# Kernel optimization log

Hardware: AMD Instinct MI355X
Metric: run time of the kernel (lower is better)

## Reference

```python
import jax, jax.numpy as jnp
import numpy as np

D_K = 64

def setup_inputs() -> dict:
    key = jax.random.key(0)
    kq, kk, kv, km = jax.random.split(key, 4)
    B, H, S, D = 8, 8, 1024, D_K
    Q = jax.random.normal(kq, (B, H, S, D), dtype=jnp.float32)
    K = jax.random.normal(kk, (B, H, S, D), dtype=jnp.float32)
    V = jax.random.normal(kv, (B, H, S, D), dtype=jnp.float32)
    attention_masks = (jax.random.uniform(km, (B, 1, 1, S)) > 0.1).astype(jnp.float32)
    return {"Q": Q, "K": K, "V": V, "attention_masks": attention_masks}

def reference(Q, K, V, attention_masks):
    # scores = exp(QK^T / sqrt(d_k))  -- raw exp, NO max-subtraction (faithful to source)
    scale = 1.0 / np.sqrt(D_K).astype(np.float32)
    scores = jnp.exp(jnp.einsum('bhqd,bhkd->bhqk', Q, K) * scale)
    scores = scores * attention_masks  # multiplicative masking
    attention_scores = scores / (jnp.sum(scores, axis=-1, keepdims=True) + 1e-8)
    context = jnp.einsum('bhqk,bhkd->bhqd', attention_scores, V)
    return (context, attention_scores)
```

## Files before the change

### kernel.cpp

```cpp
#include <hip/hip_runtime.h>


typedef float    f32x4 __attribute__((ext_vector_type(4)));
typedef _Float16 f16x8 __attribute__((ext_vector_type(8)));
typedef _Float16 f16x4 __attribute__((ext_vector_type(4)));

#define MFMA32(A, B, C) __builtin_amdgcn_mfma_f32_16x16x32_f16((A), (B), (C), 0, 0, 0)
#define MFMA16(A, B, C) __builtin_amdgcn_mfma_f32_16x16x16f16((A), (B), (C), 0, 0, 0)

#define BHN 64
#define SEQ 1024
#define DIM 64

__device__ inline f16x8 cvt8(f32x4 a, f32x4 b) {
    f16x8 r;
    r[0] = (_Float16)a[0]; r[1] = (_Float16)a[1]; r[2] = (_Float16)a[2]; r[3] = (_Float16)a[3];
    r[4] = (_Float16)b[0]; r[5] = (_Float16)b[1]; r[6] = (_Float16)b[2]; r[7] = (_Float16)b[3];
    return r;
}

__global__ __launch_bounds__(256)
void cvt_kv(const float* __restrict__ K, const float* __restrict__ V,
            _Float16* __restrict__ Kh, _Float16* __restrict__ VTP)
{
    __shared__ _Float16 tile[128 * 65];
    const int bh = blockIdx.x >> 3;
    const int kc = blockIdx.x & 7;
    const int t  = threadIdx.x;
    const size_t base = ((size_t)bh * SEQ + (size_t)kc * 128) * DIM;

    for (int it = 0; it < 8; ++it) {
        int idx = it * 256 + t;
        int key = idx >> 4;
        int c4  = idx & 15;
        f32x4 kv = *(const f32x4*)(K + base + key * DIM + c4 * 4);
        f32x4 vv = *(const f32x4*)(V + base + key * DIM + c4 * 4);
        f16x4 kh4;
        kh4[0] = (_Float16)kv[0]; kh4[1] = (_Float16)kv[1];
        kh4[2] = (_Float16)kv[2]; kh4[3] = (_Float16)kv[3];
        *(f16x4*)(Kh + base + key * DIM + c4 * 4) = kh4;
        tile[key * 65 + c4 * 4 + 0] = (_Float16)vv[0];
        tile[key * 65 + c4 * 4 + 1] = (_Float16)vv[1];
        tile[key * 65 + c4 * 4 + 2] = (_Float16)vv[2];
        tile[key * 65 + c4 * 4 + 3] = (_Float16)vv[3];
    }
    __syncthreads();
    for (int it = 0; it < 8; ++it) {
        int flat = it * 256 + t;
        int ktl  = flat >> 8;
        int rem  = flat & 255;
        int l    = rem >> 2;
        int c    = rem & 3;
        f16x4 o;
        #pragma unroll
        for (int j = 0; j < 4; ++j)
            o[j] = tile[(ktl * 16 + ((l >> 4) << 2) + j) * 65 + c * 16 + (l & 15)];
        *(f16x4*)(VTP + (((size_t)bh * 64 + kc * 8 + ktl) * 64 + l) * 16 + c * 4) = o;
    }
}

template <bool PRECONV>
__global__ __launch_bounds__(256, 2)
void attn_main(const float* __restrict__ Q, const float* __restrict__ K,
               const float* __restrict__ V, const float* __restrict__ mask,
               const _Float16* __restrict__ Kh, const _Float16* __restrict__ VTP,
               float* __restrict__ ctx, float* __restrict__ scores)
{
    __shared__ _Float16 Et[32 * 1024];

    const int bid = blockIdx.x;
    const int wg  = ((bid & 7) << 8) | (bid >> 3);
    const int bh  = wg >> 5;
    const int qb  = wg & 31;
    const int b   = bh >> 3;
    const int w    = threadIdx.x >> 6;
    const int lane = threadIdx.x & 63;
    const int col  = lane & 15;
    const int g    = lane >> 4;
    const int q0   = qb * 32;
    const int kb   = w * 256;
    const float scale = 0.125f;
    char* EtB = (char*)Et;

    f16x8 qf[2][2];
    {
        const float* qbase = Q + ((size_t)bh * SEQ + q0) * DIM;
        #pragma unroll
        for (int s = 0; s < 2; ++s)
            #pragma unroll
            for (int f = 0; f < 2; ++f) {
                const float* p = qbase + (s * 16 + col) * DIM + f * 32 + g * 8;
                qf[s][f] = cvt8(*(const f32x4*)p, *(const f32x4*)(p + 4));
            }
    }
    const float* mb = mask + (size_t)b * SEQ + kb;
    const _Float16* kbase = Kh + ((size_t)bh * SEQ + kb + col) * DIM + g * 8;
    const _Float16* vtpb  = VTP + (((size_t)bh * 64 + w * 16) * 64 + lane) * 16;

    f32x4 cacc[2][4];
    #pragma unroll
    for (int s = 0; s < 2; ++s)
        #pragma unroll
        for (int dt = 0; dt < 4; ++dt) cacc[s][dt] = (f32x4){0.f, 0.f, 0.f, 0.f};

    f16x8 k0, k1, va, vb;
    f32x4 m4;
    if (PRECONV) {
        k0 = *(const f16x8*)(kbase);
        k1 = *(const f16x8*)(kbase + 32);
        va = *(const f16x8*)(vtpb);
        vb = *(const f16x8*)(vtpb + 8);
    } else {
        const float* kp = K + ((size_t)bh * SEQ + kb + col) * DIM + g * 8;
        k0 = cvt8(*(const f32x4*)kp,        *(const f32x4*)(kp + 4));
        k1 = cvt8(*(const f32x4*)(kp + 32), *(const f32x4*)(kp + 36));
        #pragma unroll
        for (int e = 0; e < 8; ++e) {
            va[e] = (_Float16)V[((size_t)bh * SEQ + kb + g * 4 + (e & 3)) * DIM + (e >> 2) * 16 + col];
            vb[e] = (_Float16)V[((size_t)bh * SEQ + kb + g * 4 + (e & 3)) * DIM + (2 + (e >> 2)) * 16 + col];
        }
    }
    m4 = *(const f32x4*)(mb + g * 4);

    for (int kt = 0; kt < 16; ++kt) {
        const int ktn = (kt + 1) & 15;
        f16x8 n0, n1, nva, nvb;
        if (PRECONV) {
            n0  = *(const f16x8*)(kbase + (size_t)ktn * 16 * DIM);
            n1  = *(const f16x8*)(kbase + (size_t)ktn * 16 * DIM + 32);
            nva = *(const f16x8*)(vtpb + (size_t)ktn * 64 * 16);
            nvb = *(const f16x8*)(vtpb + (size_t)ktn * 64 * 16 + 8);
        } else {
            const float* kp = K + ((size_t)bh * SEQ + kb + ktn * 16 + col) * DIM + g * 8;
            n0 = cvt8(*(const f32x4*)kp,        *(const f32x4*)(kp + 4));
            n1 = cvt8(*(const f32x4*)(kp + 32), *(const f32x4*)(kp + 36));
            #pragma unroll
            for (int e = 0; e < 8; ++e) {
                nva[e] = (_Float16)V[((size_t)bh * SEQ + kb + ktn * 16 + g * 4 + (e & 3)) * DIM + (e >> 2) * 16 + col];
                nvb[e] = (_Float16)V[((size_t)bh * SEQ + kb + ktn * 16 + g * 4 + (e & 3)) * DIM + (2 + (e >> 2)) * 16 + col];
            }
        }
        f32x4 nm = *(const f32x4*)(mb + ktn * 16 + g * 4);

        f16x4 pf[2];
        #pragma unroll
        for (int s = 0; s < 2; ++s) {
            f32x4 acc = {0.f, 0.f, 0.f, 0.f};
            acc = MFMA32(k0, qf[s][0], acc);
            acc = MFMA32(k1, qf[s][1], acc);
            f16x4 eh;
            eh[0] = (_Float16)(__expf(acc[0] * scale) * m4[0]);
            eh[1] = (_Float16)(__expf(acc[1] * scale) * m4[1]);
            eh[2] = (_Float16)(__expf(acc[2] * scale) * m4[2]);
            eh[3] = (_Float16)(__expf(acc[3] * scale) * m4[3]);
            pf[s] = eh;
            const int row = s * 16 + col;
            const int kg  = (w * 64 + kt * 4 + g) ^ ((row & 3) << 2);
            *(f16x4*)(EtB + row * 2048 + kg * 8) = eh;
        }
        {
            f16x4 vt0 = __builtin_shufflevector(va, va, 0, 1, 2, 3);
            f16x4 vt1 = __builtin_shufflevector(va, va, 4, 5, 6, 7);
            f16x4 vt2 = __builtin_shufflevector(vb, vb, 0, 1, 2, 3);
            f16x4 vt3 = __builtin_shufflevector(vb, vb, 4, 5, 6, 7);
            cacc[0][0] = MFMA16(vt0, pf[0], cacc[0][0]);
            cacc[1][0] = MFMA16(vt0, pf[1], cacc[1][0]);
            cacc[0][1] = MFMA16(vt1, pf[0], cacc[0][1]);
            cacc[1][1] = MFMA16(vt1, pf[1], cacc[1][1]);
            cacc[0][2] = MFMA16(vt2, pf[0], cacc[0][2]);
            cacc[1][2] = MFMA16(vt2, pf[1], cacc[1][2]);
            cacc[0][3] = MFMA16(vt3, pf[0], cacc[0][3]);
            cacc[1][3] = MFMA16(vt3, pf[1], cacc[1][3]);
        }
        k0 = n0; k1 = n1; va = nva; vb = nvb; m4 = nm;
    }

    __syncthreads();

    const int r0 = w * 8;
    float* srow = scores + ((size_t)bh * SEQ + q0) * SEQ;
    for (int j = 0; j < 8; ++j) {
        const int r = r0 + j;
        f16x4 ev[4];
        #pragma unroll
        for (int q = 0; q < 4; ++q) {
            const int kg = (q * 64 + lane) ^ ((r & 3) << 2);
            ev[q] = *(const f16x4*)(EtB + r * 2048 + kg * 8);
        }
        float s0 = 0.f;
        #pragma unroll
        for (int q = 0; q < 4; ++q)
            #pragma unroll
            for (int i = 0; i < 4; ++i) s0 += (float)ev[q][i];
        #pragma unroll
        for (int off = 1; off < 64; off <<= 1) s0 += __shfl_xor(s0, off, 64);
        const float invr = 1.0f / (s0 + 1e-8f);
        float* dst = srow + (size_t)r * SEQ + lane * 4;
        #pragma unroll
        for (int q = 0; q < 4; ++q) {
            f32x4 o;
            o[0] = (float)ev[q][0] * invr;
            o[1] = (float)ev[q][1] * invr;
            o[2] = (float)ev[q][2] * invr;
            o[3] = (float)ev[q][3] * invr;
            __builtin_nontemporal_store(o, (f32x4*)(dst + q * 256));
        }
        if (lane == 0) *(float*)(EtB + r0 * 2048 + j * 4) = invr;
    }

    __syncthreads();

    if (w != 0) {
        float* dump = (float*)(EtB + (1 + (w - 1) * 8) * 2048);
        #pragma unroll
        for (int s = 0; s < 2; ++s)
            #pragma unroll
            for (int dt = 0; dt < 4; ++dt)
                #pragma unroll
                for (int i = 0; i < 4; ++i)
                    dump[((s * 4 + dt) * 4 + i) * 64 + lane] = cacc[s][dt][i];
    }
    __syncthreads();
    if (w == 0) {
        #pragma unroll
        for (int s = 0; s < 2; ++s) {
            const int qrow = s * 16 + col;
            const float invr = *(const float*)(EtB + (qrow >> 3) * 8 * 2048 + (qrow & 7) * 4);
            #pragma unroll
            for (int dt = 0; dt < 4; ++dt) {
                f32x4 r = cacc[s][dt];
                #pragma unroll
                for (int ww = 1; ww < 4; ++ww) {
                    const float* dump = (const float*)(EtB + (1 + (ww - 1) * 8) * 2048);
                    #pragma unroll
                    for (int i = 0; i < 4; ++i)
                        r[i] += dump[((s * 4 + dt) * 4 + i) * 64 + lane];
                }
                r[0] *= invr; r[1] *= invr; r[2] *= invr; r[3] *= invr;
                *(f32x4*)(ctx + ((size_t)bh * SEQ + q0 + qrow) * DIM + dt * 16 + g * 4) = r;
            }
        }
    }
}

extern "C" void kernel_launch(void* const* d_in, const int* in_sizes, int n_in,
                              void* d_out, int out_size, void* d_ws, size_t ws_size,
                              hipStream_t stream)
{
    const float* Q    = (const float*)d_in[0];
    const float* K    = (const float*)d_in[1];
    const float* V    = (const float*)d_in[2];
    const float* mask = (const float*)d_in[3];
    float* ctx    = (float*)d_out;
    float* scores = ctx + (size_t)BHN * SEQ * DIM;

    const size_t elems = (size_t)BHN * SEQ * DIM;
    const size_t need  = elems * 2 * sizeof(_Float16);
    if (ws_size >= need) {
        _Float16* Kh  = (_Float16*)d_ws;
        _Float16* VTP = Kh + elems;
        cvt_kv<<<512, 256, 0, stream>>>(K, V, Kh, VTP);
        attn_main<true><<<2048, 256, 0, stream>>>(Q, K, V, mask, Kh, VTP, ctx, scores);
    } else {
        attn_main<false><<<2048, 256, 0, stream>>>(Q, K, V, mask, nullptr, nullptr, ctx, scores);
    }
}
```

Before: 100.9 us.

## Give each wave full key range for 16 query rows, keep scores in registers

```diff
diff --git a/kernel.cpp b/kernel.cpp
--- a/kernel.cpp
+++ b/kernel.cpp
@@ -66,42 +66,34 @@
                const _Float16* __restrict__ Kh, const _Float16* __restrict__ VTP,
                float* __restrict__ ctx, float* __restrict__ scores)
 {
-    __shared__ _Float16 Et[32 * 1024];
-
     const int bid = blockIdx.x;
-    const int wg  = ((bid & 7) << 8) | (bid >> 3);
-    const int bh  = wg >> 5;
-    const int qb  = wg & 31;
+    const int wg  = ((bid & 7) << 7) | (bid >> 3);
+    const int bh  = wg >> 4;
+    const int qb  = wg & 15;
     const int b   = bh >> 3;
     const int w    = threadIdx.x >> 6;
     const int lane = threadIdx.x & 63;
     const int col  = lane & 15;
     const int g    = lane >> 4;
-    const int q0   = qb * 32;
-    const int kb   = w * 256;
+    const int q0   = qb * 64 + w * 16;
     const float scale = 0.125f;
-    char* EtB = (char*)Et;
-
-    f16x8 qf[2][2];
+
+    f16x8 qf0, qf1;
     {
-        const float* qbase = Q + ((size_t)bh * SEQ + q0) * DIM;
-        #pragma unroll
-        for (int s = 0; s < 2; ++s)
-            #pragma unroll
-            for (int f = 0; f < 2; ++f) {
-                const float* p = qbase + (s * 16 + col) * DIM + f * 32 + g * 8;
-                qf[s][f] = cvt8(*(const f32x4*)p, *(const f32x4*)(p + 4));
-            }
-    }
-    const float* mb = mask + (size_t)b * SEQ + kb;
-    const _Float16* kbase = Kh + ((size_t)bh * SEQ + kb + col) * DIM + g * 8;
-    const _Float16* vtpb  = VTP + (((size_t)bh * 64 + w * 16) * 64 + lane) * 16;
-
-    f32x4 cacc[2][4];
+        const float* p = Q + ((size_t)bh * SEQ + q0 + col) * DIM + g * 8;
+        qf0 = cvt8(*(const f32x4*)p,        *(const f32x4*)(p + 4));
+        qf1 = cvt8(*(const f32x4*)(p + 32), *(const f32x4*)(p + 36));
+    }
+    const float* mb = mask + (size_t)b * SEQ;
+    const _Float16* kbase = Kh + ((size_t)bh * SEQ + col) * DIM + g * 8;
+    const _Float16* vtpb  = VTP + ((size_t)bh * 64 * 64 + lane) * 16;
+
+    f32x4 cacc[4];
     #pragma unroll
-    for (int s = 0; s < 2; ++s)
-        #pragma unroll
-        for (int dt = 0; dt < 4; ++dt) cacc[s][dt] = (f32x4){0.f, 0.f, 0.f, 0.f};
+    for (int dt = 0; dt < 4; ++dt) cacc[dt] = (f32x4){0.f, 0.f, 0.f, 0.f};
+
+    f16x4 E[64];
+    float rsum = 0.f;
 
     f16x8 k0, k1, va, vb;
     f32x4 m4;
@@ -111,19 +103,20 @@
         va = *(const f16x8*)(vtpb);
         vb = *(const f16x8*)(vtpb + 8);
     } else {
-        const float* kp = K + ((size_t)bh * SEQ + kb + col) * DIM + g * 8;
+        const float* kp = K + ((size_t)bh * SEQ + col) * DIM + g * 8;
         k0 = cvt8(*(const f32x4*)kp,        *(const f32x4*)(kp + 4));
         k1 = cvt8(*(const f32x4*)(kp + 32), *(const f32x4*)(kp + 36));
         #pragma unroll
         for (int e = 0; e < 8; ++e) {
-            va[e] = (_Float16)V[((size_t)bh * SEQ + kb + g * 4 + (e & 3)) * DIM + (e >> 2) * 16 + col];
-            vb[e] = (_Float16)V[((size_t)bh * SEQ + kb + g * 4 + (e & 3)) * DIM + (2 + (e >> 2)) * 16 + col];
+            va[e] = (_Float16)V[((size_t)bh * SEQ + g * 4 + (e & 3)) * DIM + (e >> 2) * 16 + col];
+            vb[e] = (_Float16)V[((size_t)bh * SEQ + g * 4 + (e & 3)) * DIM + (2 + (e >> 2)) * 16 + col];
         }
     }
     m4 = *(const f32x4*)(mb + g * 4);
 
-    for (int kt = 0; kt < 16; ++kt) {
-        const int ktn = (kt + 1) & 15;
+    #pragma unroll
+    for (int kt = 0; kt < 64; ++kt) {
+        const int ktn = (kt + 1) & 63;
         f16x8 n0, n1, nva, nvb;
         if (PRECONV) {
             n0  = *(const f16x8*)(kbase + (size_t)ktn * 16 * DIM);
@@ -131,115 +124,65 @@
             nva = *(const f16x8*)(vtpb + (size_t)ktn * 64 * 16);
             nvb = *(const f16x8*)(vtpb + (size_t)ktn * 64 * 16 + 8);
         } else {
-            const float* kp = K + ((size_t)bh * SEQ + kb + ktn * 16 + col) * DIM + g * 8;
+            const float* kp = K + ((size_t)bh * SEQ + ktn * 16 + col) * DIM + g * 8;
             n0 = cvt8(*(const f32x4*)kp,        *(const f32x4*)(kp + 4));
             n1 = cvt8(*(const f32x4*)(kp + 32), *(const f32x4*)(kp + 36));
             #pragma unroll
             for (int e = 0; e < 8; ++e) {
-                nva[e] = (_Float16)V[((size_t)bh * SEQ + kb + ktn * 16 + g * 4 + (e & 3)) * DIM + (e >> 2) * 16 + col];
-                nvb[e] = (_Float16)V[((size_t)bh * SEQ + kb + ktn * 16 + g * 4 + (e & 3)) * DIM + (2 + (e >> 2)) * 16 + col];
+                nva[e] = (_Float16)V[((size_t)bh * SEQ + ktn * 16 + g * 4 + (e & 3)) * DIM + (e >> 2) * 16 + col];
+                nvb[e] = (_Float16)V[((size_t)bh * SEQ + ktn * 16 + g * 4 + (e & 3)) * DIM + (2 + (e >> 2)) * 16 + col];
             }
         }
         f32x4 nm = *(const f32x4*)(mb + ktn * 16 + g * 4);
 
-        f16x4 pf[2];
-        #pragma unroll
-        for (int s = 0; s < 2; ++s) {
-            f32x4 acc = {0.f, 0.f, 0.f, 0.f};
-            acc = MFMA32(k0, qf[s][0], acc);
-            acc = MFMA32(k1, qf[s][1], acc);
-            f16x4 eh;
-            eh[0] = (_Float16)(__expf(acc[0] * scale) * m4[0]);
-            eh[1] = (_Float16)(__expf(acc[1] * scale) * m4[1]);
-            eh[2] = (_Float16)(__expf(acc[2] * scale) * m4[2]);
-            eh[3] = (_Float16)(__expf(acc[3] * scale) * m4[3]);
-            pf[s] = eh;
-            const int row = s * 16 + col;
-            const int kg  = (w * 64 + kt * 4 + g) ^ ((row & 3) << 2);
-            *(f16x4*)(EtB + row * 2048 + kg * 8) = eh;
-        }
+        f32x4 acc = {0.f, 0.f, 0.f, 0.f};
+        acc = MFMA32(k0, qf0, acc);
+        acc = MFMA32(k1, qf1, acc);
+        const float e0 = __expf(acc[0] * scale) * m4[0];
+        const float e1 = __expf(acc[1] * scale) * m4[1];
+        const float e2 = __expf(acc[2] * scale) * m4[2];
+        const float e3 = __expf(acc[3] * scale) * m4[3];
+        rsum += e0 + e1 + e2 + e3;
+        f16x4 pf;
+        pf[0] = (_Float16)e0; pf[1] = (_Float16)e1;
+        pf[2] = (_Float16)e2; pf[3] = (_Float16)e3;
+        E[kt] = pf;
+
         {
             f16x4 vt0 = __builtin_shufflevector(va, va, 0, 1, 2, 3);
             f16x4 vt1 = __builtin_shufflevector(va, va, 4, 5, 6, 7);
             f16x4 vt2 = __builtin_shufflevector(vb, vb, 0, 1, 2, 3);
             f16x4 vt3 = __builtin_shufflevector(vb, vb, 4, 5, 6, 7);
-            cacc[0][0] = MFMA16(vt0, pf[0], cacc[0][0]);
-            cacc[1][0] = MFMA16(vt0, pf[1], cacc[1][0]);
-            cacc[0][1] = MFMA16(vt1, pf[0], cacc[0][1]);
-            cacc[1][1] = MFMA16(vt1, pf[1], cacc[1][1]);
-            cacc[0][2] = MFMA16(vt2, pf[0], cacc[0][2]);
-            cacc[1][2] = MFMA16(vt2, pf[1], cacc[1][2]);
-            cacc[0][3] = MFMA16(vt3, pf[0], cacc[0][3]);
-            cacc[1][3] = MFMA16(vt3, pf[1], cacc[1][3]);
+            cacc[0] = MFMA16(vt0, pf, cacc[0]);
+            cacc[1] = MFMA16(vt1, pf, cacc[1]);
+            cacc[2] = MFMA16(vt2, pf, cacc[2]);
+            cacc[3] = MFMA16(vt3, pf, cacc[3]);
         }
         k0 = n0; k1 = n1; va = nva; vb = nvb; m4 = nm;
     }
 
-    __syncthreads();
-
-    const int r0 = w * 8;
-    float* srow = scores + ((size_t)bh * SEQ + q0) * SEQ;
-    for (int j = 0; j < 8; ++j) {
-        const int r = r0 + j;
-        f16x4 ev[4];
+    rsum += __shfl_xor(rsum, 16, 64);
+    rsum += __shfl_xor(rsum, 32, 64);
+    const float inv = 1.0f / (rsum + 1e-8f);
+
+    {
+        float* srow = scores + ((size_t)bh * SEQ + q0 + col) * SEQ + g * 4;
         #pragma unroll
-        for (int q = 0; q < 4; ++q) {
-            const int kg = (q * 64 + lane) ^ ((r & 3) << 2);
-            ev[q] = *(const f16x4*)(EtB + r * 2048 + kg * 8);
-        }
-        float s0 = 0.f;
-        #pragma unroll
-        for (int q = 0; q < 4; ++q)
-            #pragma unroll
-            for (int i = 0; i < 4; ++i) s0 += (float)ev[q][i];
-        #pragma unroll
-        for (int off = 1; off < 64; off <<= 1) s0 += __shfl_xor(s0, off, 64);
-        const float invr = 1.0f / (s0 + 1e-8f);
-        float* dst = srow + (size_t)r * SEQ + lane * 4;
-        #pragma unroll
-        for (int q = 0; q < 4; ++q) {
+        for (int kt = 0; kt < 64; ++kt) {
             f32x4 o;
-            o[0] = (float)ev[q][0] * invr;
-            o[1] = (float)ev[q][1] * invr;
-            o[2] = (float)ev[q][2] * invr;
-            o[3] = (float)ev[q][3] * invr;
-            __builtin_nontemporal_store(o, (f32x4*)(dst + q * 256));
-        }
-        if (lane == 0) *(float*)(EtB + r0 * 2048 + j * 4) = invr;
-    }
-
-    __syncthreads();
-
-    if (w != 0) {
-        float* dump = (float*)(EtB + (1 + (w - 1) * 8) * 2048);
-        #pragma unroll
-        for (int s = 0; s < 2; ++s)
-            #pragma unroll
-            for (int dt = 0; dt < 4; ++dt)
-                #pragma unroll
-                for (int i = 0; i < 4; ++i)
-                    dump[((s * 4 + dt) * 4 + i) * 64 + lane] = cacc[s][dt][i];
-    }
-    __syncthreads();
-    if (w == 0) {
-        #pragma unroll
-        for (int s = 0; s < 2; ++s) {
-            const int qrow = s * 16 + col;
-            const float invr = *(const float*)(EtB + (qrow >> 3) * 8 * 2048 + (qrow & 7) * 4);
-            #pragma unroll
-            for (int dt = 0; dt < 4; ++dt) {
-                f32x4 r = cacc[s][dt];
-                #pragma unroll
-                for (int ww = 1; ww < 4; ++ww) {
-                    const float* dump = (const float*)(EtB + (1 + (ww - 1) * 8) * 2048);
-                    #pragma unroll
-                    for (int i = 0; i < 4; ++i)
-                        r[i] += dump[((s * 4 + dt) * 4 + i) * 64 + lane];
-                }
-                r[0] *= invr; r[1] *= invr; r[2] *= invr; r[3] *= invr;
-                *(f32x4*)(ctx + ((size_t)bh * SEQ + q0 + qrow) * DIM + dt * 16 + g * 4) = r;
-            }
-        }
+            o[0] = (float)E[kt][0] * inv;
+            o[1] = (float)E[kt][1] * inv;
+            o[2] = (float)E[kt][2] * inv;
+            o[3] = (float)E[kt][3] * inv;
+            __builtin_nontemporal_store(o, (f32x4*)(srow + kt * 16));
+        }
+    }
+
+    #pragma unroll
+    for (int dt = 0; dt < 4; ++dt) {
+        f32x4 r = cacc[dt];
+        r[0] *= inv; r[1] *= inv; r[2] *= inv; r[3] *= inv;
+        *(f32x4*)(ctx + ((size_t)bh * SEQ + q0 + col) * DIM + dt * 16 + g * 4) = r;
     }
 }
 
@@ -260,8 +203,8 @@
         _Float16* Kh  = (_Float16*)d_ws;
         _Float16* VTP = Kh + elems;
         cvt_kv<<<512, 256, 0, stream>>>(K, V, Kh, VTP);
-        attn_main<true><<<2048, 256, 0, stream>>>(Q, K, V, mask, Kh, VTP, ctx, scores);
+        attn_main<true><<<1024, 256, 0, stream>>>(Q, K, V, mask, Kh, VTP, ctx, scores);
     } else {
-        attn_main<false><<<2048, 256, 0, stream>>>(Q, K, V, mask, nullptr, nullptr, ctx, scores);
-    }
-}
+        attn_main<false><<<1024, 256, 0, stream>>>(Q, K, V, mask, nullptr, nullptr, ctx, scores);
+    }
+}
```

New measurement: 270.4 us. +168.1%, slower.

## Accumulate row sums in registers during QK loop and double-buffer K/V prefetch

Applied to the files above, without the earlier changes.

```diff
diff --git a/kernel.cpp b/kernel.cpp
--- a/kernel.cpp
+++ b/kernel.cpp
@@ -67,6 +67,7 @@
                float* __restrict__ ctx, float* __restrict__ scores)
 {
     __shared__ _Float16 Et[32 * 1024];
+    __shared__ float rs[4][2][16];
 
     const int bid = blockIdx.x;
     const int wg  = ((bid & 7) << 8) | (bid >> 3);
@@ -102,99 +103,104 @@
     for (int s = 0; s < 2; ++s)
         #pragma unroll
         for (int dt = 0; dt < 4; ++dt) cacc[s][dt] = (f32x4){0.f, 0.f, 0.f, 0.f};
-
-    f16x8 k0, k1, va, vb;
-    f32x4 m4;
-    if (PRECONV) {
-        k0 = *(const f16x8*)(kbase);
-        k1 = *(const f16x8*)(kbase + 32);
-        va = *(const f16x8*)(vtpb);
-        vb = *(const f16x8*)(vtpb + 8);
-    } else {
-        const float* kp = K + ((size_t)bh * SEQ + kb + col) * DIM + g * 8;
-        k0 = cvt8(*(const f32x4*)kp,        *(const f32x4*)(kp + 4));
-        k1 = cvt8(*(const f32x4*)(kp + 32), *(const f32x4*)(kp + 36));
-        #pragma unroll
-        for (int e = 0; e < 8; ++e) {
-            va[e] = (_Float16)V[((size_t)bh * SEQ + kb + g * 4 + (e & 3)) * DIM + (e >> 2) * 16 + col];
-            vb[e] = (_Float16)V[((size_t)bh * SEQ + kb + g * 4 + (e & 3)) * DIM + (2 + (e >> 2)) * 16 + col];
-        }
-    }
-    m4 = *(const f32x4*)(mb + g * 4);
-
-    for (int kt = 0; kt < 16; ++kt) {
-        const int ktn = (kt + 1) & 15;
-        f16x8 n0, n1, nva, nvb;
+    float rsum[2] = {0.f, 0.f};
+
+    auto loadS = [&](int kt, f16x8& a, f16x8& c, f16x8& x, f16x8& y, f32x4& m) {
         if (PRECONV) {
-            n0  = *(const f16x8*)(kbase + (size_t)ktn * 16 * DIM);
-            n1  = *(const f16x8*)(kbase + (size_t)ktn * 16 * DIM + 32);
-            nva = *(const f16x8*)(vtpb + (size_t)ktn * 64 * 16);
-            nvb = *(const f16x8*)(vtpb + (size_t)ktn * 64 * 16 + 8);
+            a = *(const f16x8*)(kbase + (size_t)kt * 16 * DIM);
+            c = *(const f16x8*)(kbase + (size_t)kt * 16 * DIM + 32);
+            x = *(const f16x8*)(vtpb + (size_t)kt * 64 * 16);
+            y = *(const f16x8*)(vtpb + (size_t)kt * 64 * 16 + 8);
         } else {
-            const float* kp = K + ((size_t)bh * SEQ + kb + ktn * 16 + col) * DIM + g * 8;
-            n0 = cvt8(*(const f32x4*)kp,        *(const f32x4*)(kp + 4));
-            n1 = cvt8(*(const f32x4*)(kp + 32), *(const f32x4*)(kp + 36));
+            const float* kp = K + ((size_t)bh * SEQ + kb + kt * 16 + col) * DIM + g * 8;
+            a = cvt8(*(const f32x4*)kp,        *(const f32x4*)(kp + 4));
+            c = cvt8(*(const f32x4*)(kp + 32), *(const f32x4*)(kp + 36));
             #pragma unroll
             for (int e = 0; e < 8; ++e) {
-                nva[e] = (_Float16)V[((size_t)bh * SEQ + kb + ktn * 16 + g * 4 + (e & 3)) * DIM + (e >> 2) * 16 + col];
-                nvb[e] = (_Float16)V[((size_t)bh * SEQ + kb + ktn * 16 + g * 4 + (e & 3)) * DIM + (2 + (e >> 2)) * 16 + col];
+                x[e] = (_Float16)V[((size_t)bh * SEQ + kb + kt * 16 + g * 4 + (e & 3)) * DIM + (e >> 2) * 16 + col];
+                y[e] = (_Float16)V[((size_t)bh * SEQ + kb + kt * 16 + g * 4 + (e & 3)) * DIM + (2 + (e >> 2)) * 16 + col];
             }
         }
-        f32x4 nm = *(const f32x4*)(mb + ktn * 16 + g * 4);
-
+        m = *(const f32x4*)(mb + kt * 16 + g * 4);
+    };
+
+    auto body = [&](int kt, f16x8 k0, f16x8 k1, f16x8 va, f16x8 vb, f32x4 m4) {
         f16x4 pf[2];
         #pragma unroll
         for (int s = 0; s < 2; ++s) {
             f32x4 acc = {0.f, 0.f, 0.f, 0.f};
             acc = MFMA32(k0, qf[s][0], acc);
             acc = MFMA32(k1, qf[s][1], acc);
+            const float e0 = __expf(acc[0] * scale) * m4[0];
+            const float e1 = __expf(acc[1] * scale) * m4[1];
+            const float e2 = __expf(acc[2] * scale) * m4[2];
+            const float e3 = __expf(acc[3] * scale) * m4[3];
+            rsum[s] += e0 + e1 + e2 + e3;
             f16x4 eh;
-            eh[0] = (_Float16)(__expf(acc[0] * scale) * m4[0]);
-            eh[1] = (_Float16)(__expf(acc[1] * scale) * m4[1]);
-            eh[2] = (_Float16)(__expf(acc[2] * scale) * m4[2]);
-            eh[3] = (_Float16)(__expf(acc[3] * scale) * m4[3]);
+            eh[0] = (_Float16)e0; eh[1] = (_Float16)e1;
+            eh[2] = (_Float16)e2; eh[3] = (_Float16)e3;
             pf[s] = eh;
             const int row = s * 16 + col;
             const int kg  = (w * 64 + kt * 4 + g) ^ ((row & 3) << 2);
             *(f16x4*)(EtB + row * 2048 + kg * 8) = eh;
         }
-        {
-            f16x4 vt0 = __builtin_shufflevector(va, va, 0, 1, 2, 3);
-            f16x4 vt1 = __builtin_shufflevector(va, va, 4, 5, 6, 7);
-            f16x4 vt2 = __builtin_shufflevector(vb, vb, 0, 1, 2, 3);
-            f16x4 vt3 = __builtin_shufflevector(vb, vb, 4, 5, 6, 7);
-            cacc[0][0] = MFMA16(vt0, pf[0], cacc[0][0]);
-            cacc[1][0] = MFMA16(vt0, pf[1], cacc[1][0]);
-            cacc[0][1] = MFMA16(vt1, pf[0], cacc[0][1]);
-            cacc[1][1] = MFMA16(vt1, pf[1], cacc[1][1]);
-            cacc[0][2] = MFMA16(vt2, pf[0], cacc[0][2]);
-            cacc[1][2] = MFMA16(vt2, pf[1], cacc[1][2]);
-            cacc[0][3] = MFMA16(vt3, pf[0], cacc[0][3]);
-            cacc[1][3] = MFMA16(vt3, pf[1], cacc[1][3]);
-        }
-        k0 = n0; k1 = n1; va = nva; vb = nvb; m4 = nm;
-    }
-
+        f16x4 vt0 = __builtin_shufflevector(va, va, 0, 1, 2, 3);
+        f16x4 vt1 = __builtin_shufflevector(va, va, 4, 5, 6, 7);
+        f16x4 vt2 = __builtin_shufflevector(vb, vb, 0, 1, 2, 3);
+        f16x4 vt3 = __builtin_shufflevector(vb, vb, 4, 5, 6, 7);
+        cacc[0][0] = MFMA16(vt0, pf[0], cacc[0][0]);
+        cacc[1][0] = MFMA16(vt0, pf[1], cacc[1][0]);
+        cacc[0][1] = MFMA16(vt1, pf[0], cacc[0][1]);
+        cacc[1][1] = MFMA16(vt1, pf[1], cacc[1][1]);
+        cacc[0][2] = MFMA16(vt2, pf[0], cacc[0][2]);
+        cacc[1][2] = MFMA16(vt2, pf[1], cacc[1][2]);
+        cacc[0][3] = MFMA16(vt3, pf[0], cacc[0][3]);
+        cacc[1][3] = MFMA16(vt3, pf[1], cacc[1][3]);
+    };
+
+    f16x8 k0A, k1A, vaA, vbA, k0B, k1B, vaB, vbB;
+    f32x4 m4A, m4B;
+    loadS(0, k0A, k1A, vaA, vbA, m4A);
+    loadS(1, k0B, k1B, vaB, vbB, m4B);
+
+    #pragma unroll 1
+    for (int kt = 0; kt < 16; kt += 2) {
+        f16x8 n0, n1, nx, ny;
+        f32x4 nm;
+        loadS((kt + 2) & 15, n0, n1, nx, ny, nm);
+        body(kt, k0A, k1A, vaA, vbA, m4A);
+        k0A = n0; k1A = n1; vaA = nx; vbA = ny; m4A = nm;
+
+        loadS((kt + 3) & 15, n0, n1, nx, ny, nm);
+        body(kt + 1, k0B, k1B, vaB, vbB, m4B);
+        k0B = n0; k1B = n1; vaB = nx; vbB = ny; m4B = nm;
+    }
+
+    #pragma unroll
+    for (int s = 0; s < 2; ++s) {
+        float r = rsum[s];
+        r += __shfl_xor(r, 16, 64);
+        r += __shfl_xor(r, 32, 64);
+        rsum[s] = r;
+    }
+    if (g == 0) {
+        rs[w][0][col] = rsum[0];
+        rs[w][1][col] = rsum[1];
+    }
     __syncthreads();
 
     const int r0 = w * 8;
     float* srow = scores + ((size_t)bh * SEQ + q0) * SEQ;
     for (int j = 0; j < 8; ++j) {
-        const int r = r0 + j;
+        const int r  = r0 + j;
+        const int si = r >> 4, ci = r & 15;
+        const float invr = 1.0f / (rs[0][si][ci] + rs[1][si][ci] + rs[2][si][ci] + rs[3][si][ci] + 1e-8f);
         f16x4 ev[4];
         #pragma unroll
         for (int q = 0; q < 4; ++q) {
             const int kg = (q * 64 + lane) ^ ((r & 3) << 2);
             ev[q] = *(const f16x4*)(EtB + r * 2048 + kg * 8);
         }
-        float s0 = 0.f;
-        #pragma unroll
-        for (int q = 0; q < 4; ++q)
-            #pragma unroll
-            for (int i = 0; i < 4; ++i) s0 += (float)ev[q][i];
-        #pragma unroll
-        for (int off = 1; off < 64; off <<= 1) s0 += __shfl_xor(s0, off, 64);
-        const float invr = 1.0f / (s0 + 1e-8f);
         float* dst = srow + (size_t)r * SEQ + lane * 4;
         #pragma unroll
         for (int q = 0; q < 4; ++q) {
@@ -205,39 +211,38 @@
             o[3] = (float)ev[q][3] * invr;
             __builtin_nontemporal_store(o, (f32x4*)(dst + q * 256));
         }
-        if (lane == 0) *(float*)(EtB + r0 * 2048 + j * 4) = invr;
-    }
-
-    __syncthreads();
-
+    }
+
+    __syncthreads();
+
+    float* dumpf = (float*)Et;
     if (w != 0) {
-        float* dump = (float*)(EtB + (1 + (w - 1) * 8) * 2048);
+        float* d = dumpf + (w - 1) * 2048;
         #pragma unroll
         for (int s = 0; s < 2; ++s)
             #pragma unroll
             for (int dt = 0; dt < 4; ++dt)
                 #pragma unroll
                 for (int i = 0; i < 4; ++i)
-                    dump[((s * 4 + dt) * 4 + i) * 64 + lane] = cacc[s][dt][i];
+                    d[((s * 4 + dt) * 4 + i) * 64 + lane] = cacc[s][dt][i];
     }
     __syncthreads();
     if (w == 0) {
         #pragma unroll
         for (int s = 0; s < 2; ++s) {
-            const int qrow = s * 16 + col;
-            const float invr = *(const float*)(EtB + (qrow >> 3) * 8 * 2048 + (qrow & 7) * 4);
+            const float invs = 1.0f / (rs[0][s][col] + rs[1][s][col] + rs[2][s][col] + rs[3][s][col] + 1e-8f);
             #pragma unroll
             for (int dt = 0; dt < 4; ++dt) {
                 f32x4 r = cacc[s][dt];
                 #pragma unroll
-                for (int ww = 1; ww < 4; ++ww) {
-                    const float* dump = (const float*)(EtB + (1 + (ww - 1) * 8) * 2048);
+                for (int ww = 0; ww < 3; ++ww) {
+                    const float* d = dumpf + ww * 2048;
                     #pragma unroll
                     for (int i = 0; i < 4; ++i)
-                        r[i] += dump[((s * 4 + dt) * 4 + i) * 64 + lane];
+                        r[i] += d[((s * 4 + dt) * 4 + i) * 64 + lane];
                 }
-                r[0] *= invr; r[1] *= invr; r[2] *= invr; r[3] *= invr;
-                *(f32x4*)(ctx + ((size_t)bh * SEQ + q0 + qrow) * DIM + dt * 16 + g * 4) = r;
+                r[0] *= invs; r[1] *= invs; r[2] *= invs; r[3] *= invs;
+                *(f32x4*)(ctx + ((size_t)bh * SEQ + q0 + s * 16 + col) * DIM + dt * 16 + g * 4) = r;
             }
         }
     }
```

Result: faster. 93.83 us (-7.0%).
